# Kernel tuning notes

Measured on AMD Instinct MI355X. Metric: run time of the kernel, lower is better.

The kernel has to match this reference:

```python
import jax, jax.numpy as jnp
import numpy as np

NUM_EXPERTS = 8
HIDDEN = 2048
INTER = 4096
TOKENS = 8192  # divisible by NUM_EXPERTS


def setup_inputs() -> dict:
    key = jax.random.key(0)
    k1, k2, k3 = jax.random.split(key, 3)
    hidden_states = jax.random.normal(k1, (TOKENS, HIDDEN), dtype=jnp.float32)
    gate_up_proj = jax.random.normal(k2, (NUM_EXPERTS, HIDDEN, 2 * INTER), dtype=jnp.float32) * 0.02
    down_proj = jax.random.normal(k3, (NUM_EXPERTS, INTER, HIDDEN), dtype=jnp.float32) * 0.02
    return {"hidden_states": hidden_states, "gate_up_proj": gate_up_proj, "down_proj": down_proj}


def reference(hidden_states, gate_up_proj, down_proj):
    E, H = gate_up_proj.shape[0], gate_up_proj.shape[1]
    x = hidden_states.reshape(E, -1, H)                      # (E, T/E, H)
    gate_up = jnp.einsum('eth,ehf->etf', x, gate_up_proj)    # (E, T/E, 2I)
    gate, up = jnp.split(gate_up, 2, axis=-1)
    acted = up * jax.nn.silu(gate)                           # (E, T/E, I)
    out = jnp.einsum('eti,eih->eth', acted, down_proj)       # (E, T/E, H)
    return out.reshape(-1, H)
```

## Files before the change

### kernel.cpp

```cpp
#include <hip/hip_runtime.h>


#define E_   8
#define H_   2048
#define I_   4096
#define T_   8192
#define TPE  1024

typedef __bf16 bf16x8 __attribute__((ext_vector_type(8)));
typedef float  f32x4  __attribute__((ext_vector_type(4)));

__device__ __forceinline__ unsigned short f2bf(float f) {
  union { float f; unsigned int u; } v; v.f = f;
  unsigned int u = v.u;
  u += 0x7FFFu + ((u >> 16) & 1u);
  return (unsigned short)(u >> 16);
}

__device__ __forceinline__ void async16(const void* g, void* l) {
  __builtin_amdgcn_global_load_lds(
      (__attribute__((address_space(1))) void*)(g),
      (__attribute__((address_space(3))) void*)(l), 16, 0, 0);
}

#define SB0()      __builtin_amdgcn_sched_barrier(0)
#define BAR()      __builtin_amdgcn_s_barrier()
#define WAITLGKM() asm volatile("s_waitcnt lgkmcnt(0)" ::: "memory")
#define WAITVM(n)  asm volatile("s_waitcnt vmcnt(" #n ")" ::: "memory")

__global__ void convert_bf16(const float* __restrict__ src,
                             unsigned short* __restrict__ dst, long n) {
  long i = ((long)blockIdx.x * blockDim.x + threadIdx.x) * 4;
  const long stride = (long)gridDim.x * blockDim.x * 4;
  for (; i < n; i += stride) {
    const float4 v = *(const float4*)&src[i];
    ushort4 o;
    o.x = f2bf(v.x); o.y = f2bf(v.y); o.z = f2bf(v.z); o.w = f2bf(v.w);
    *(ushort4*)&dst[i] = o;
  }
}

template <int K, int NBN, int LDB, bool SILU>
__global__ __launch_bounds__(512, 2)
void gemm_fused(const unsigned short* __restrict__ Aall,
                const float* __restrict__ Ball,
                void* __restrict__ Cout,
                long sA, long sB, long sC) {
  extern __shared__ char smem[];
  constexpr int NT = K / 64;

  const int tid  = threadIdx.x;
  const int wave = tid >> 6;
  const int lane = tid & 63;
  const int lr   = lane & 15;
  const int lq   = lane >> 4;
  const int wid_m = wave >> 2;
  const int wid_n = wave & 3;

  const int nwg = gridDim.x;
  const int bid = blockIdx.x;
  const int wg  = (bid & 7) * (nwg >> 3) + (bid >> 3);
  const int mb  = wg & 3;
  const int tmp = wg >> 2;
  const int nb  = tmp % NBN;
  const int e   = tmp / NBN;

  const unsigned short* A = Aall + (long)e * sA + (long)(mb * 256) * K;
  const float*          B = Ball + (long)e * sB;

  const int stl  = tid >> 3;
  const int scol = ((tid & 7) ^ (stl & 7)) * 8;

  auto stageA = [&](int bi, int q, int kt) {
    const long col = (long)kt * 64 + scol;
    char* l0 = smem + bi * 32768 + q * 16384 + wave * 1024;
    async16(A + (long)(q * 64 + stl) * K + col,        l0);
    async16(A + (long)(128 + q * 64 + stl) * K + col,  l0 + 8192);
  };

  int colq;
  {
    const int st = 4 * lane;
    const int b  = st >> 7;
    const int r  = st & 127;
    const int w  = r >> 5;
    const int nf = (r >> 4) & 1;
    const int l4 = st & 15;
    if (SILU) colq = nb * 128 + (w * 32 + b * 16 + l4) + (nf ? I_ : 0);
    else      colq = nb * 256 + w * 64 + (b * 2 + nf) * 16 + l4;
  }
  const float* Bq = B + colq;

  f32x4 bv[8];
  auto LOADB = [&](int kt) {
    const long kbase = (long)kt * 64 + wave * 8;
#pragma unroll
    for (int i = 0; i < 8; ++i)
      bv[i] = *(const f32x4*)&Bq[(kbase + i) * (long)LDB];
  };
  auto WRITEB = [&](int bo) {
    char* LBw = smem + 65536 + bo * 32768;
    const int slot = wave ^ (lane & 7);
#pragma unroll
    for (int j = 0; j < 4; ++j) {
      bf16x8 pk;
#pragma unroll
      for (int i = 0; i < 8; ++i) pk[i] = (__bf16)bv[i][j];
      const int st = 4 * lane + j;
      *(bf16x8*)(LBw + st * 128 + slot * 16) = pk;
    }
  };

  const int axA0 = ((0 + lq) ^ (lr & 7)) * 16;
  const int axA1 = ((4 + lq) ^ (lr & 7)) * 16;
  const int bxn[2] = { (lr >> 2), 4 + (lr >> 2) };

  f32x4 acc[8][4];
#pragma unroll
  for (int m = 0; m < 8; ++m)
#pragma unroll
    for (int n = 0; n < 4; ++n) acc[m][n] = (f32x4)0.0f;

  const int t1p = (NT > 1) ? 1 : 0;
  LOADB(0);
  stageA(0, 0, 0);
  stageA(0, 1, 0);
  SB0();
  WAITVM(4); SB0();
  WRITEB(0);
  WAITLGKM(); SB0();
  stageA(1, 0, t1p); SB0();
  LOADB(t1p); SB0();
  stageA(1, 1, t1p); SB0();
  WAITVM(12); SB0();
  BAR();

#pragma unroll 1
  for (int t = 0; t < NT; ++t) {
    const int cur = t & 1;
    const int bo  = cur ^ 1;
    const char* LA = smem + cur * 32768;
    const char* LB = smem + 65536 + cur * 32768;
    const int t2v = (t + 2 < NT) ? t + 2 : NT - 1;

    bf16x8 a[4][2], b0[2][2], b1[2][2];

#pragma unroll
    for (int mf = 0; mf < 4; ++mf) {
      const int st = wid_m * 64 + mf * 16 + lr;
      a[mf][0] = *(const bf16x8*)(LA + st * 128 + axA0);
      a[mf][1] = *(const bf16x8*)(LA + st * 128 + axA1);
    }
#pragma unroll
    for (int nf = 0; nf < 2; ++nf) {
      const int st = wid_n * 32 + nf * 16 + lr;
      b0[nf][0] = *(const bf16x8*)(LB + st * 128 + ((0 + lq) ^ bxn[nf]) * 16);
      b0[nf][1] = *(const bf16x8*)(LB + st * 128 + ((4 + lq) ^ bxn[nf]) * 16);
    }
    SB0();
    BAR();
    WAITLGKM(); SB0();
    __builtin_amdgcn_s_setprio(1);
#pragma unroll
    for (int mf = 0; mf < 4; ++mf)
#pragma unroll
      for (int nf = 0; nf < 2; ++nf) {
        acc[mf][nf] = __builtin_amdgcn_mfma_f32_16x16x32_bf16(a[mf][0], b0[nf][0], acc[mf][nf], 0, 0, 0);
        acc[mf][nf] = __builtin_amdgcn_mfma_f32_16x16x32_bf16(a[mf][1], b0[nf][1], acc[mf][nf], 0, 0, 0);
      }
    __builtin_amdgcn_s_setprio(0);
    BAR();

#pragma unroll
    for (int nf = 0; nf < 2; ++nf) {
      const int st = 128 + wid_n * 32 + nf * 16 + lr;
      b1[nf][0] = *(const bf16x8*)(LB + st * 128 + ((0 + lq) ^ bxn[nf]) * 16);
      b1[nf][1] = *(const bf16x8*)(LB + st * 128 + ((4 + lq) ^ bxn[nf]) * 16);
    }
    stageA(cur, 0, t2v);
    SB0();
    BAR();
    WAITLGKM(); SB0();
    __builtin_amdgcn_s_setprio(1);
#pragma unroll
    for (int mf = 0; mf < 4; ++mf)
#pragma unroll
      for (int nf = 0; nf < 2; ++nf) {
        acc[mf][2 + nf] = __builtin_amdgcn_mfma_f32_16x16x32_bf16(a[mf][0], b1[nf][0], acc[mf][2 + nf], 0, 0, 0);
        acc[mf][2 + nf] = __builtin_amdgcn_mfma_f32_16x16x32_bf16(a[mf][1], b1[nf][1], acc[mf][2 + nf], 0, 0, 0);
      }
    __builtin_amdgcn_s_setprio(0);
    BAR();

#pragma unroll
    for (int mf = 0; mf < 4; ++mf) {
      const int st = 128 + wid_m * 64 + mf * 16 + lr;
      a[mf][0] = *(const bf16x8*)(LA + st * 128 + axA0);
      a[mf][1] = *(const bf16x8*)(LA + st * 128 + axA1);
    }
    SB0();
    WAITVM(4); SB0();
    WRITEB(bo);
    WAITLGKM(); SB0();
    LOADB(t2v);
    SB0();
    BAR();
    __builtin_amdgcn_s_setprio(1);
#pragma unroll
    for (int mf = 0; mf < 4; ++mf)
#pragma unroll
      for (int nf = 0; nf < 2; ++nf) {
        acc[4 + mf][2 + nf] = __builtin_amdgcn_mfma_f32_16x16x32_bf16(a[mf][0], b1[nf][0], acc[4 + mf][2 + nf], 0, 0, 0);
        acc[4 + mf][2 + nf] = __builtin_amdgcn_mfma_f32_16x16x32_bf16(a[mf][1], b1[nf][1], acc[4 + mf][2 + nf], 0, 0, 0);
      }
    __builtin_amdgcn_s_setprio(0);
    BAR();

    stageA(cur, 1, t2v);
    SB0();
    WAITVM(12); SB0();
    BAR();
    __builtin_amdgcn_s_setprio(1);
#pragma unroll
    for (int mf = 0; mf < 4; ++mf)
#pragma unroll
      for (int nf = 0; nf < 2; ++nf) {
        acc[4 + mf][nf] = __builtin_amdgcn_mfma_f32_16x16x32_bf16(a[mf][0], b0[nf][0], acc[4 + mf][nf], 0, 0, 0);
        acc[4 + mf][nf] = __builtin_amdgcn_mfma_f32_16x16x32_bf16(a[mf][1], b0[nf][1], acc[4 + mf][nf], 0, 0, 0);
      }
    __builtin_amdgcn_s_setprio(0);
    BAR();
  }

  WAITVM(0);

  if (SILU) {
    unsigned short* Cc = (unsigned short*)Cout + (long)e * sC;
#pragma unroll
    for (int mf = 0; mf < 8; ++mf)
#pragma unroll
      for (int p = 0; p < 2; ++p)
#pragma unroll
        for (int rr = 0; rr < 4; ++rr) {
          const int row = mb * 256 + wid_m * 128 + mf * 16 + lq * 4 + rr;
          const int col = nb * 128 + wid_n * 32 + p * 16 + lr;
          const float g = acc[mf][p * 2][rr];
          const float u = acc[mf][p * 2 + 1][rr];
          Cc[(long)row * I_ + col] = f2bf(u * (g / (1.0f + __expf(-g))));
        }
  } else {
    float* Cc = (float*)Cout + (long)e * sC;
#pragma unroll
    for (int mf = 0; mf < 8; ++mf)
#pragma unroll
      for (int q = 0; q < 4; ++q)
#pragma unroll
        for (int rr = 0; rr < 4; ++rr) {
          const int row = mb * 256 + wid_m * 128 + mf * 16 + lq * 4 + rr;
          const int col = nb * 256 + wid_n * 64 + q * 16 + lr;
          Cc[(long)row * H_ + col] = acc[mf][q][rr];
        }
  }
}

extern "C" void kernel_launch(void* const* d_in, const int* in_sizes, int n_in,
                              void* d_out, int out_size, void* d_ws, size_t ws_size,
                              hipStream_t stream) {
  const float* hs = (const float*)d_in[0];
  const float* w1 = (const float*)d_in[1];
  const float* w2 = (const float*)d_in[2];
  float* out = (float*)d_out;
  char* ws = (char*)d_ws;

  const long HB_B  = (long)T_ * H_ * 2;
  const long ACT_B = (long)T_ * I_ * 2;
  if (ws_size < (size_t)(HB_B + ACT_B)) return;

  unsigned short* hiddenB = (unsigned short*)(ws);
  unsigned short* acted   = (unsigned short*)(ws + HB_B);

  hipLaunchKernelGGL(convert_bf16, dim3(2048), dim3(256), 0, stream,
                     hs, hiddenB, (long)T_ * H_);

  hipLaunchKernelGGL((gemm_fused<H_, 32, 2 * I_, true>),
                     dim3(1024), dim3(512), 131072, stream,
                     hiddenB, w1, acted,
                     (long)TPE * H_, (long)H_ * 2 * I_, (long)TPE * I_);

  hipLaunchKernelGGL((gemm_fused<I_, 8, H_, false>),
                     dim3(256), dim3(512), 131072, stream,
                     acted, w2, out,
                     (long)TPE * I_, (long)I_ * H_, (long)TPE * H_);
}
```

Baseline: 525.2 us.

## Double-buffer B register staging and unroll main loop by two

Splits the B prefetch registers into two alternating sets, so the next tile's global load can be issued right after the current set is converted and written to LDS, without waiting on the LDS write. The main loop is unrolled by two to swap the register sets, and the wait/barrier is moved after the load issue. The B LDS swizzle is changed to key on the stored row instead of the lane, which lets the A and B read offsets share the same XOR pattern. This costs 32 more VGPRs of live B data, which may hurt occupancy under the 512x2 launch bounds.

Result: slower. 604.6 us (+15.1%).

```diff
diff --git a/kernel.cpp b/kernel.cpp
--- a/kernel.cpp
+++ b/kernel.cpp
@@ -48,6 +48,7 @@
                 long sA, long sB, long sC) {
   extern __shared__ char smem[];
   constexpr int NT = K / 64;
+  static_assert(NT % 2 == 0, "NT must be even for the x2 unroll");
 
   const int tid  = threadIdx.x;
   const int wave = tid >> 6;
@@ -91,29 +92,29 @@
   }
   const float* Bq = B + colq;
 
-  f32x4 bv[8];
-  auto LOADB = [&](int kt) {
+  f32x4 bvA[8], bvB[8];
+
+  auto LOADB = [&](auto& bv, int kt) {
     const long kbase = (long)kt * 64 + wave * 8;
 #pragma unroll
     for (int i = 0; i < 8; ++i)
       bv[i] = *(const f32x4*)&Bq[(kbase + i) * (long)LDB];
   };
-  auto WRITEB = [&](int bo) {
+  auto WRITEB = [&](int bo, auto& bv) {
     char* LBw = smem + 65536 + bo * 32768;
-    const int slot = wave ^ (lane & 7);
 #pragma unroll
     for (int j = 0; j < 4; ++j) {
       bf16x8 pk;
 #pragma unroll
       for (int i = 0; i < 8; ++i) pk[i] = (__bf16)bv[i][j];
-      const int st = 4 * lane + j;
+      const int st   = 4 * lane + j;
+      const int slot = wave ^ (st & 7);
       *(bf16x8*)(LBw + st * 128 + slot * 16) = pk;
     }
   };
 
-  const int axA0 = ((0 + lq) ^ (lr & 7)) * 16;
-  const int axA1 = ((4 + lq) ^ (lr & 7)) * 16;
-  const int bxn[2] = { (lr >> 2), 4 + (lr >> 2) };
+  const int ax0 = ((0 + lq) ^ (lr & 7)) * 16;
+  const int ax1 = ((4 + lq) ^ (lr & 7)) * 16;
 
   f32x4 acc[8][4];
 #pragma unroll
@@ -122,21 +123,20 @@
     for (int n = 0; n < 4; ++n) acc[m][n] = (f32x4)0.0f;
 
   const int t1p = (NT > 1) ? 1 : 0;
-  LOADB(0);
+  LOADB(bvA, 0);
   stageA(0, 0, 0);
   stageA(0, 1, 0);
   SB0();
   WAITVM(4); SB0();
-  WRITEB(0);
+  WRITEB(0, bvA);
   WAITLGKM(); SB0();
   stageA(1, 0, t1p); SB0();
-  LOADB(t1p); SB0();
+  LOADB(bvB, t1p); SB0();
   stageA(1, 1, t1p); SB0();
   WAITVM(12); SB0();
   BAR();
 
-#pragma unroll 1
-  for (int t = 0; t < NT; ++t) {
+  auto body = [&](int t, auto& bvW, auto& bvL) {
     const int cur = t & 1;
     const int bo  = cur ^ 1;
     const char* LA = smem + cur * 32768;
@@ -148,14 +148,14 @@
 #pragma unroll
     for (int mf = 0; mf < 4; ++mf) {
       const int st = wid_m * 64 + mf * 16 + lr;
-      a[mf][0] = *(const bf16x8*)(LA + st * 128 + axA0);
-      a[mf][1] = *(const bf16x8*)(LA + st * 128 + axA1);
+      a[mf][0] = *(const bf16x8*)(LA + st * 128 + ax0);
+      a[mf][1] = *(const bf16x8*)(LA + st * 128 + ax1);
     }
 #pragma unroll
     for (int nf = 0; nf < 2; ++nf) {
       const int st = wid_n * 32 + nf * 16 + lr;
-      b0[nf][0] = *(const bf16x8*)(LB + st * 128 + ((0 + lq) ^ bxn[nf]) * 16);
-      b0[nf][1] = *(const bf16x8*)(LB + st * 128 + ((4 + lq) ^ bxn[nf]) * 16);
+      b0[nf][0] = *(const bf16x8*)(LB + st * 128 + ax0);
+      b0[nf][1] = *(const bf16x8*)(LB + st * 128 + ax1);
     }
     SB0();
     BAR();
@@ -174,8 +174,8 @@
 #pragma unroll
     for (int nf = 0; nf < 2; ++nf) {
       const int st = 128 + wid_n * 32 + nf * 16 + lr;
-      b1[nf][0] = *(const bf16x8*)(LB + st * 128 + ((0 + lq) ^ bxn[nf]) * 16);
-      b1[nf][1] = *(const bf16x8*)(LB + st * 128 + ((4 + lq) ^ bxn[nf]) * 16);
+      b1[nf][0] = *(const bf16x8*)(LB + st * 128 + ax0);
+      b1[nf][1] = *(const bf16x8*)(LB + st * 128 + ax1);
     }
     stageA(cur, 0, t2v);
     SB0();
@@ -195,16 +195,16 @@
 #pragma unroll
     for (int mf = 0; mf < 4; ++mf) {
       const int st = 128 + wid_m * 64 + mf * 16 + lr;
-      a[mf][0] = *(const bf16x8*)(LA + st * 128 + axA0);
-      a[mf][1] = *(const bf16x8*)(LA + st * 128 + axA1);
+      a[mf][0] = *(const bf16x8*)(LA + st * 128 + ax0);
+      a[mf][1] = *(const bf16x8*)(LA + st * 128 + ax1);
     }
     SB0();
     WAITVM(4); SB0();
-    WRITEB(bo);
+    WRITEB(bo, bvW);
+    LOADB(bvL, t2v);
+    SB0();
+    BAR();
     WAITLGKM(); SB0();
-    LOADB(t2v);
-    SB0();
-    BAR();
     __builtin_amdgcn_s_setprio(1);
 #pragma unroll
     for (int mf = 0; mf < 4; ++mf)
@@ -230,6 +230,12 @@
       }
     __builtin_amdgcn_s_setprio(0);
     BAR();
+  };
+
+#pragma unroll 1
+  for (int tt = 0; tt < NT; tt += 2) {
+    body(tt,     bvB, bvA);
+    body(tt + 1, bvA, bvB);
   }
 
   WAITVM(0);
```

## Shrink GEMM block tile to 128x128 with 256 threads and permuted B columns

Applied to the files above, without the earlier changes.

Both expert GEMMs now use 128x128 output tiles computed by 4 waves instead of 256x256 tiles by 8 waves. This halves LDS use (64 KB) and quadruples the grid, which gives more workgroups per CU and better load balance. The B staging layout changes and a lane column permutation (pcol) is added so B fragment reads and output columns match. The cost is less operand reuse per tile, so each block does more global traffic per FLOP, and the f32 B loads and conversion become a larger share of the work.

Result: slower. 683.7 us (+30.2%).

```diff
diff --git a/kernel.cpp b/kernel.cpp
--- a/kernel.cpp
+++ b/kernel.cpp
@@ -41,7 +41,7 @@
 }
 
 template <int K, int NBN, int LDB, bool SILU>
-__global__ __launch_bounds__(512, 2)
+__global__ __launch_bounds__(256, 2)
 void gemm_fused(const unsigned short* __restrict__ Aall,
                 const float* __restrict__ Ball,
                 void* __restrict__ Cout,
@@ -54,18 +54,19 @@
   const int lane = tid & 63;
   const int lr   = lane & 15;
   const int lq   = lane >> 4;
-  const int wid_m = wave >> 2;
-  const int wid_n = wave & 3;
+  const int wid_m = wave >> 1;
+  const int wid_n = wave & 1;
+  const int pcol  = ((lr & 3) << 2) | (lr >> 2);
 
   const int nwg = gridDim.x;
   const int bid = blockIdx.x;
   const int wg  = (bid & 7) * (nwg >> 3) + (bid >> 3);
-  const int mb  = wg & 3;
-  const int tmp = wg >> 2;
+  const int mb  = wg & 7;
+  const int tmp = wg >> 3;
   const int nb  = tmp % NBN;
   const int e   = tmp / NBN;
 
-  const unsigned short* A = Aall + (long)e * sA + (long)(mb * 256) * K;
+  const unsigned short* A = Aall + (long)e * sA + (long)(mb * 128) * K;
   const float*          B = Ball + (long)e * sB;
 
   const int stl  = tid >> 3;
@@ -73,53 +74,58 @@
 
   auto stageA = [&](int bi, int q, int kt) {
     const long col = (long)kt * 64 + scol;
-    char* l0 = smem + bi * 32768 + q * 16384 + wave * 1024;
-    async16(A + (long)(q * 64 + stl) * K + col,        l0);
-    async16(A + (long)(128 + q * 64 + stl) * K + col,  l0 + 8192);
-  };
-
+    char* l0 = smem + bi * 16384 + q * 4096 + wave * 1024;
+    async16(A + (long)(q * 32 + stl) * K + col,       l0);
+    async16(A + (long)(64 + q * 32 + stl) * K + col,  l0 + 8192);
+  };
+
+  const int quad = tid & 31;
+  const int koB  = tid >> 5;
   int colq;
   {
-    const int st = 4 * lane;
-    const int b  = st >> 7;
-    const int r  = st & 127;
-    const int w  = r >> 5;
-    const int nf = (r >> 4) & 1;
-    const int l4 = st & 15;
-    if (SILU) colq = nb * 128 + (w * 32 + b * 16 + l4) + (nf ? I_ : 0);
-    else      colq = nb * 256 + w * 64 + (b * 2 + nf) * 16 + l4;
+    const int st = 4 * quad;
+    if (SILU) {
+      colq = nb * 64 + (st >> 5) * 16 + (st & 15) + (((st >> 4) & 1) ? I_ : 0);
+    } else {
+      colq = nb * 128 + st;
+    }
   }
   const float* Bq = B + colq;
 
   f32x4 bv[8];
   auto LOADB = [&](int kt) {
-    const long kbase = (long)kt * 64 + wave * 8;
+    const long kbase = (long)kt * 64 + koB * 8;
 #pragma unroll
     for (int i = 0; i < 8; ++i)
       bv[i] = *(const f32x4*)&Bq[(kbase + i) * (long)LDB];
   };
   auto WRITEB = [&](int bo) {
-    char* LBw = smem + 65536 + bo * 32768;
-    const int slot = wave ^ (lane & 7);
+    char* LBw = smem + 32768 + bo * 16384;
+    const int slot = koB ^ (quad & 7);
 #pragma unroll
     for (int j = 0; j < 4; ++j) {
       bf16x8 pk;
 #pragma unroll
       for (int i = 0; i < 8; ++i) pk[i] = (__bf16)bv[i][j];
-      const int st = 4 * lane + j;
+      const int st = 4 * quad + j;
       *(bf16x8*)(LBw + st * 128 + slot * 16) = pk;
     }
   };
 
   const int axA0 = ((0 + lq) ^ (lr & 7)) * 16;
   const int axA1 = ((4 + lq) ^ (lr & 7)) * 16;
-  const int bxn[2] = { (lr >> 2), 4 + (lr >> 2) };
-
-  f32x4 acc[8][4];
-#pragma unroll
-  for (int m = 0; m < 8; ++m)
+
+  f32x4 acc[4][4];
+#pragma unroll
+  for (int m = 0; m < 4; ++m)
 #pragma unroll
     for (int n = 0; n < 4; ++n) acc[m][n] = (f32x4)0.0f;
+
+  auto readB = [&](const char* LB, int nf, int ks) -> bf16x8 {
+    const int st = wid_n * 64 + nf * 16 + pcol;
+    const int sl = ((ks * 4 + lq) ^ ((st >> 2) & 7)) * 16;
+    return *(const bf16x8*)(LB + st * 128 + sl);
+  };
 
   const int t1p = (NT > 1) ? 1 : 0;
   LOADB(0);
@@ -139,43 +145,41 @@
   for (int t = 0; t < NT; ++t) {
     const int cur = t & 1;
     const int bo  = cur ^ 1;
-    const char* LA = smem + cur * 32768;
-    const char* LB = smem + 65536 + cur * 32768;
+    const char* LA = smem + cur * 16384;
+    const char* LB = smem + 32768 + cur * 16384;
     const int t2v = (t + 2 < NT) ? t + 2 : NT - 1;
 
-    bf16x8 a[4][2], b0[2][2], b1[2][2];
-
-#pragma unroll
-    for (int mf = 0; mf < 4; ++mf) {
+    bf16x8 aLo[2][2], aHi[2][2], bLo[2][2], bHi[2][2];
+
+#pragma unroll
+    for (int mf = 0; mf < 2; ++mf) {
       const int st = wid_m * 64 + mf * 16 + lr;
-      a[mf][0] = *(const bf16x8*)(LA + st * 128 + axA0);
-      a[mf][1] = *(const bf16x8*)(LA + st * 128 + axA1);
+      aLo[mf][0] = *(const bf16x8*)(LA + st * 128 + axA0);
+      aLo[mf][1] = *(const bf16x8*)(LA + st * 128 + axA1);
     }
 #pragma unroll
     for (int nf = 0; nf < 2; ++nf) {
-      const int st = wid_n * 32 + nf * 16 + lr;
-      b0[nf][0] = *(const bf16x8*)(LB + st * 128 + ((0 + lq) ^ bxn[nf]) * 16);
-      b0[nf][1] = *(const bf16x8*)(LB + st * 128 + ((4 + lq) ^ bxn[nf]) * 16);
+      bLo[nf][0] = readB(LB, nf, 0);
+      bLo[nf][1] = readB(LB, nf, 1);
     }
     SB0();
     BAR();
     WAITLGKM(); SB0();
     __builtin_amdgcn_s_setprio(1);
 #pragma unroll
-    for (int mf = 0; mf < 4; ++mf)
-#pragma unroll
-      for (int nf = 0; nf < 2; ++nf) {
-        acc[mf][nf] = __builtin_amdgcn_mfma_f32_16x16x32_bf16(a[mf][0], b0[nf][0], acc[mf][nf], 0, 0, 0);
-        acc[mf][nf] = __builtin_amdgcn_mfma_f32_16x16x32_bf16(a[mf][1], b0[nf][1], acc[mf][nf], 0, 0, 0);
+    for (int mf = 0; mf < 2; ++mf)
+#pragma unroll
+      for (int nf = 0; nf < 2; ++nf) {
+        acc[mf][nf] = __builtin_amdgcn_mfma_f32_16x16x32_bf16(aLo[mf][0], bLo[nf][0], acc[mf][nf], 0, 0, 0);
+        acc[mf][nf] = __builtin_amdgcn_mfma_f32_16x16x32_bf16(aLo[mf][1], bLo[nf][1], acc[mf][nf], 0, 0, 0);
       }
     __builtin_amdgcn_s_setprio(0);
     BAR();
 
 #pragma unroll
     for (int nf = 0; nf < 2; ++nf) {
-      const int st = 128 + wid_n * 32 + nf * 16 + lr;
-      b1[nf][0] = *(const bf16x8*)(LB + st * 128 + ((0 + lq) ^ bxn[nf]) * 16);
-      b1[nf][1] = *(const bf16x8*)(LB + st * 128 + ((4 + lq) ^ bxn[nf]) * 16);
+      bHi[nf][0] = readB(LB, 2 + nf, 0);
+      bHi[nf][1] = readB(LB, 2 + nf, 1);
     }
     stageA(cur, 0, t2v);
     SB0();
@@ -183,20 +187,20 @@
     WAITLGKM(); SB0();
     __builtin_amdgcn_s_setprio(1);
 #pragma unroll
-    for (int mf = 0; mf < 4; ++mf)
-#pragma unroll
-      for (int nf = 0; nf < 2; ++nf) {
-        acc[mf][2 + nf] = __builtin_amdgcn_mfma_f32_16x16x32_bf16(a[mf][0], b1[nf][0], acc[mf][2 + nf], 0, 0, 0);
-        acc[mf][2 + nf] = __builtin_amdgcn_mfma_f32_16x16x32_bf16(a[mf][1], b1[nf][1], acc[mf][2 + nf], 0, 0, 0);
-      }
-    __builtin_amdgcn_s_setprio(0);
-    BAR();
-
-#pragma unroll
-    for (int mf = 0; mf < 4; ++mf) {
-      const int st = 128 + wid_m * 64 + mf * 16 + lr;
-      a[mf][0] = *(const bf16x8*)(LA + st * 128 + axA0);
-      a[mf][1] = *(const bf16x8*)(LA + st * 128 + axA1);
+    for (int mf = 0; mf < 2; ++mf)
+#pragma unroll
+      for (int nf = 0; nf < 2; ++nf) {
+        acc[mf][2 + nf] = __builtin_amdgcn_mfma_f32_16x16x32_bf16(aLo[mf][0], bHi[nf][0], acc[mf][2 + nf], 0, 0, 0);
+        acc[mf][2 + nf] = __builtin_amdgcn_mfma_f32_16x16x32_bf16(aLo[mf][1], bHi[nf][1], acc[mf][2 + nf], 0, 0, 0);
+      }
+    __builtin_amdgcn_s_setprio(0);
+    BAR();
+
+#pragma unroll
+    for (int mf = 0; mf < 2; ++mf) {
+      const int st = wid_m * 64 + 32 + mf * 16 + lr;
+      aHi[mf][0] = *(const bf16x8*)(LA + st * 128 + axA0);
+      aHi[mf][1] = *(const bf16x8*)(LA + st * 128 + axA1);
     }
     SB0();
     WAITVM(4); SB0();
@@ -207,11 +211,11 @@
     BAR();
     __builtin_amdgcn_s_setprio(1);
 #pragma unroll
-    for (int mf = 0; mf < 4; ++mf)
-#pragma unroll
-      for (int nf = 0; nf < 2; ++nf) {
-        acc[4 + mf][2 + nf] = __builtin_amdgcn_mfma_f32_16x16x32_bf16(a[mf][0], b1[nf][0], acc[4 + mf][2 + nf], 0, 0, 0);
-        acc[4 + mf][2 + nf] = __builtin_amdgcn_mfma_f32_16x16x32_bf16(a[mf][1], b1[nf][1], acc[4 + mf][2 + nf], 0, 0, 0);
+    for (int mf = 0; mf < 2; ++mf)
+#pragma unroll
+      for (int nf = 0; nf < 2; ++nf) {
+        acc[2 + mf][2 + nf] = __builtin_amdgcn_mfma_f32_16x16x32_bf16(aHi[mf][0], bHi[nf][0], acc[2 + mf][2 + nf], 0, 0, 0);
+        acc[2 + mf][2 + nf] = __builtin_amdgcn_mfma_f32_16x16x32_bf16(aHi[mf][1], bHi[nf][1], acc[2 + mf][2 + nf], 0, 0, 0);
       }
     __builtin_amdgcn_s_setprio(0);
     BAR();
@@ -222,11 +226,11 @@
     BAR();
     __builtin_amdgcn_s_setprio(1);
 #pragma unroll
-    for (int mf = 0; mf < 4; ++mf)
-#pragma unroll
-      for (int nf = 0; nf < 2; ++nf) {
-        acc[4 + mf][nf] = __builtin_amdgcn_mfma_f32_16x16x32_bf16(a[mf][0], b0[nf][0], acc[4 + mf][nf], 0, 0, 0);
-        acc[4 + mf][nf] = __builtin_amdgcn_mfma_f32_16x16x32_bf16(a[mf][1], b0[nf][1], acc[4 + mf][nf], 0, 0, 0);
+    for (int mf = 0; mf < 2; ++mf)
+#pragma unroll
+      for (int nf = 0; nf < 2; ++nf) {
+        acc[2 + mf][nf] = __builtin_amdgcn_mfma_f32_16x16x32_bf16(aHi[mf][0], bLo[nf][0], acc[2 + mf][nf], 0, 0, 0);
+        acc[2 + mf][nf] = __builtin_amdgcn_mfma_f32_16x16x32_bf16(aHi[mf][1], bLo[nf][1], acc[2 + mf][nf], 0, 0, 0);
       }
     __builtin_amdgcn_s_setprio(0);
     BAR();
@@ -237,13 +241,13 @@
   if (SILU) {
     unsigned short* Cc = (unsigned short*)Cout + (long)e * sC;
 #pragma unroll
-    for (int mf = 0; mf < 8; ++mf)
+    for (int mf = 0; mf < 4; ++mf)
 #pragma unroll
       for (int p = 0; p < 2; ++p)
 #pragma unroll
         for (int rr = 0; rr < 4; ++rr) {
-          const int row = mb * 256 + wid_m * 128 + mf * 16 + lq * 4 + rr;
-          const int col = nb * 128 + wid_n * 32 + p * 16 + lr;
+          const int row = mb * 128 + wid_m * 64 + mf * 16 + lq * 4 + rr;
+          const int col = nb * 64 + wid_n * 32 + p * 16 + pcol;
           const float g = acc[mf][p * 2][rr];
           const float u = acc[mf][p * 2 + 1][rr];
           Cc[(long)row * I_ + col] = f2bf(u * (g / (1.0f + __expf(-g))));
@@ -251,14 +255,14 @@
   } else {
     float* Cc = (float*)Cout + (long)e * sC;
 #pragma unroll
-    for (int mf = 0; mf < 8; ++mf)
-#pragma unroll
-      for (int q = 0; q < 4; ++q)
+    for (int mf = 0; mf < 4; ++mf)
+#pragma unroll
+      for (int nf = 0; nf < 4; ++nf)
 #pragma unroll
         for (int rr = 0; rr < 4; ++rr) {
-          const int row = mb * 256 + wid_m * 128 + mf * 16 + lq * 4 + rr;
-          const int col = nb * 256 + wid_n * 64 + q * 16 + lr;
-          Cc[(long)row * H_ + col] = acc[mf][q][rr];
+          const int row = mb * 128 + wid_m * 64 + mf * 16 + lq * 4 + rr;
+          const int col = nb * 128 + wid_n * 64 + nf * 16 + pcol;
+          Cc[(long)row * H_ + col] = acc[mf][nf][rr];
         }
   }
 }
@@ -282,13 +286,13 @@
   hipLaunchKernelGGL(convert_bf16, dim3(2048), dim3(256), 0, stream,
                      hs, hiddenB, (long)T_ * H_);
 
-  hipLaunchKernelGGL((gemm_fused<H_, 32, 2 * I_, true>),
-                     dim3(1024), dim3(512), 131072, stream,
+  hipLaunchKernelGGL((gemm_fused<H_, 64, 2 * I_, true>),
+                     dim3(4096), dim3(256), 65536, stream,
                      hiddenB, w1, acted,
                      (long)TPE * H_, (long)H_ * 2 * I_, (long)TPE * I_);
 
-  hipLaunchKernelGGL((gemm_fused<I_, 8, H_, false>),
-                     dim3(256), dim3(512), 131072, stream,
+  hipLaunchKernelGGL((gemm_fused<I_, 16, H_, false>),
+                     dim3(1024), dim3(256), 65536, stream,
                      acted, w2, out,
                      (long)TPE * I_, (long)I_ * H_, (long)TPE * H_);
 }
```

## Make first GEMM persistent over multiple N tiles per workgroup

Applied to the files above, without the earlier changes.

The gate/up GEMM launch drops from 1024 to 256 workgroups, and each workgroup now loops over 4 consecutive N-tiles. The software pipeline runs continuously across tile boundaries, and an epilogue writes and resets the accumulators between tiles. The aim is to cut the wave-quantization tail and the pipeline prologue/drain overhead of launching many short workgroups. In exchange, the epilogue stores now sit inside the main loop and can stall the pipeline. The mid-loop A prefetch also reloads the same A rows for each tile, so A is not reused across tiles.

After: 792.8 us. +51.0%, slower.

```diff
diff --git a/kernel.cpp b/kernel.cpp
--- a/kernel.cpp
+++ b/kernel.cpp
@@ -40,14 +40,15 @@
   }
 }
 
-template <int K, int NBN, int LDB, bool SILU>
+template <int K, int NBL, int NBN, int LDB, bool SILU>
 __global__ __launch_bounds__(512, 2)
 void gemm_fused(const unsigned short* __restrict__ Aall,
                 const float* __restrict__ Ball,
                 void* __restrict__ Cout,
                 long sA, long sB, long sC) {
   extern __shared__ char smem[];
-  constexpr int NT = K / 64;
+  constexpr int NT  = K / 64;
+  constexpr int TTN = NT * NBL;
 
   const int tid  = threadIdx.x;
   const int wave = tid >> 6;
@@ -60,10 +61,11 @@
   const int nwg = gridDim.x;
   const int bid = blockIdx.x;
   const int wg  = (bid & 7) * (nwg >> 3) + (bid >> 3);
+  constexpr int NBG = NBN / NBL;
   const int mb  = wg & 3;
-  const int tmp = wg >> 2;
-  const int nb  = tmp % NBN;
-  const int e   = tmp / NBN;
+  const int nbg = (wg >> 2) % NBG;
+  const int e   = wg / (4 * NBG);
+  const int nb0 = nbg * NBL;
 
   const unsigned short* A = Aall + (long)e * sA + (long)(mb * 256) * K;
   const float*          B = Ball + (long)e * sB;
@@ -71,14 +73,15 @@
   const int stl  = tid >> 3;
   const int scol = ((tid & 7) ^ (stl & 7)) * 8;
 
-  auto stageA = [&](int bi, int q, int kt) {
+  auto stageA = [&](int bi, int q, int ttArg) {
+    const int  kt  = ttArg % NT;
     const long col = (long)kt * 64 + scol;
     char* l0 = smem + bi * 32768 + q * 16384 + wave * 1024;
     async16(A + (long)(q * 64 + stl) * K + col,        l0);
     async16(A + (long)(128 + q * 64 + stl) * K + col,  l0 + 8192);
   };
 
-  int colq;
+  int colq0;
   {
     const int st = 4 * lane;
     const int b  = st >> 7;
@@ -86,17 +89,21 @@
     const int w  = r >> 5;
     const int nf = (r >> 4) & 1;
     const int l4 = st & 15;
-    if (SILU) colq = nb * 128 + (w * 32 + b * 16 + l4) + (nf ? I_ : 0);
-    else      colq = nb * 256 + w * 64 + (b * 2 + nf) * 16 + l4;
+    if (SILU) colq0 = nb0 * 128 + (w * 32 + b * 16 + l4) + (nf ? I_ : 0);
+    else      colq0 = nb0 * 256 + w * 64 + (b * 2 + nf) * 16 + l4;
   }
-  const float* Bq = B + colq;
+  const float* Bq = B + colq0;
+  constexpr int NBSTEP = SILU ? 128 : 256;
 
   f32x4 bv[8];
-  auto LOADB = [&](int kt) {
+  auto LOADB = [&](int ttArg) {
+    const int  nbi   = ttArg / NT;
+    const int  kt    = ttArg % NT;
     const long kbase = (long)kt * 64 + wave * 8;
+    const float* p   = Bq + nbi * NBSTEP;
 #pragma unroll
     for (int i = 0; i < 8; ++i)
-      bv[i] = *(const f32x4*)&Bq[(kbase + i) * (long)LDB];
+      bv[i] = *(const f32x4*)&p[(kbase + i) * (long)LDB];
   };
   auto WRITEB = [&](int bo) {
     char* LBw = smem + 65536 + bo * 32768;
@@ -121,7 +128,41 @@
 #pragma unroll
     for (int n = 0; n < 4; ++n) acc[m][n] = (f32x4)0.0f;
 
-  const int t1p = (NT > 1) ? 1 : 0;
+  auto epilogue = [&](int nbi) {
+    const int nb = nb0 + nbi;
+    if (SILU) {
+      unsigned short* Cc = (unsigned short*)Cout + (long)e * sC;
+#pragma unroll
+      for (int mf = 0; mf < 8; ++mf)
+#pragma unroll
+        for (int p = 0; p < 2; ++p)
+#pragma unroll
+          for (int rr = 0; rr < 4; ++rr) {
+            const int row = mb * 256 + wid_m * 128 + mf * 16 + lq * 4 + rr;
+            const int col = nb * 128 + wid_n * 32 + p * 16 + lr;
+            const float g = acc[mf][p * 2][rr];
+            const float u = acc[mf][p * 2 + 1][rr];
+            Cc[(long)row * I_ + col] = f2bf(u * (g / (1.0f + __expf(-g))));
+          }
+    } else {
+      float* Cc = (float*)Cout + (long)e * sC;
+#pragma unroll
+      for (int mf = 0; mf < 8; ++mf)
+#pragma unroll
+        for (int q = 0; q < 4; ++q)
+#pragma unroll
+          for (int rr = 0; rr < 4; ++rr) {
+            const int row = mb * 256 + wid_m * 128 + mf * 16 + lq * 4 + rr;
+            const int col = nb * 256 + wid_n * 64 + q * 16 + lr;
+            Cc[(long)row * H_ + col] = acc[mf][q][rr];
+          }
+    }
+#pragma unroll
+    for (int m = 0; m < 8; ++m)
+#pragma unroll
+      for (int n = 0; n < 4; ++n) acc[m][n] = (f32x4)0.0f;
+  };
+
   LOADB(0);
   stageA(0, 0, 0);
   stageA(0, 1, 0);
@@ -129,19 +170,18 @@
   WAITVM(4); SB0();
   WRITEB(0);
   WAITLGKM(); SB0();
-  stageA(1, 0, t1p); SB0();
-  LOADB(t1p); SB0();
-  stageA(1, 1, t1p); SB0();
+  stageA(1, 0, 1); SB0();
+  LOADB(1); SB0();
+  stageA(1, 1, 1); SB0();
   WAITVM(12); SB0();
   BAR();
 
-#pragma unroll 1
-  for (int t = 0; t < NT; ++t) {
-    const int cur = t & 1;
+  auto body = [&](int tt) {
+    const int cur = tt & 1;
     const int bo  = cur ^ 1;
     const char* LA = smem + cur * 32768;
     const char* LB = smem + 65536 + cur * 32768;
-    const int t2v = (t + 2 < NT) ? t + 2 : NT - 1;
+    const int t2v = (tt + 2 < TTN) ? tt + 2 : TTN - 1;
 
     bf16x8 a[4][2], b0[2][2], b1[2][2];
 
@@ -230,37 +270,17 @@
       }
     __builtin_amdgcn_s_setprio(0);
     BAR();
+  };
+
+#pragma unroll 1
+  for (int tt = 0; tt < TTN; tt += 2) {
+    body(tt);
+    body(tt + 1);
+    if (((tt + 1) % NT) == NT - 1)
+      epilogue((tt + 1) / NT);
   }
 
   WAITVM(0);
-
-  if (SILU) {
-    unsigned short* Cc = (unsigned short*)Cout + (long)e * sC;
-#pragma unroll
-    for (int mf = 0; mf < 8; ++mf)
-#pragma unroll
-      for (int p = 0; p < 2; ++p)
-#pragma unroll
-        for (int rr = 0; rr < 4; ++rr) {
-          const int row = mb * 256 + wid_m * 128 + mf * 16 + lq * 4 + rr;
-          const int col = nb * 128 + wid_n * 32 + p * 16 + lr;
-          const float g = acc[mf][p * 2][rr];
-          const float u = acc[mf][p * 2 + 1][rr];
-          Cc[(long)row * I_ + col] = f2bf(u * (g / (1.0f + __expf(-g))));
-        }
-  } else {
-    float* Cc = (float*)Cout + (long)e * sC;
-#pragma unroll
-    for (int mf = 0; mf < 8; ++mf)
-#pragma unroll
-      for (int q = 0; q < 4; ++q)
-#pragma unroll
-        for (int rr = 0; rr < 4; ++rr) {
-          const int row = mb * 256 + wid_m * 128 + mf * 16 + lq * 4 + rr;
-          const int col = nb * 256 + wid_n * 64 + q * 16 + lr;
-          Cc[(long)row * H_ + col] = acc[mf][q][rr];
-        }
-  }
 }
 
 extern "C" void kernel_launch(void* const* d_in, const int* in_sizes, int n_in,
@@ -282,12 +302,12 @@
   hipLaunchKernelGGL(convert_bf16, dim3(2048), dim3(256), 0, stream,
                      hs, hiddenB, (long)T_ * H_);
 
-  hipLaunchKernelGGL((gemm_fused<H_, 32, 2 * I_, true>),
-                     dim3(1024), dim3(512), 131072, stream,
+  hipLaunchKernelGGL((gemm_fused<H_, 4, 32, 2 * I_, true>),
+                     dim3(256), dim3(512), 131072, stream,
                      hiddenB, w1, acted,
                      (long)TPE * H_, (long)H_ * 2 * I_, (long)TPE * I_);
 
-  hipLaunchKernelGGL((gemm_fused<I_, 8, H_, false>),
+  hipLaunchKernelGGL((gemm_fused<I_, 1, 8, H_, false>),
                      dim3(256), dim3(512), 131072, stream,
                      acted, w2, out,
                      (long)TPE * I_, (long)I_ * H_, (long)TPE * H_);
```
